# Performance work log

Hardware: AMD Instinct MI355X
Metric: run time of the kernel (lower is better)

Reference implementation:

```python
import jax, jax.numpy as jnp
import numpy as np

B, N, F_IN, F_OUT = 8, 2048, 256, 128
ALPHA = 0.2  # LeakyReLU negative slope
NEG_BIG = -9e15


def setup_inputs() -> dict:
    key = jax.random.key(0)
    k1, k2, k3, k4 = jax.random.split(key, 4)
    h = jax.random.normal(k1, (B, N, F_IN), dtype=jnp.float32)
    adj = jax.random.randint(k2, (B, N, N), 0, 2, dtype=jnp.int32)
    W = jax.random.normal(k3, (F_IN, F_OUT), dtype=jnp.float32) * 0.05
    a = jax.random.normal(k4, (2 * F_OUT,), dtype=jnp.float32) * 0.05
    return {"h": h, "adj": adj, "W": W, "a": a}


def reference(h, adj, W, a):
    # Wh: [B, N, F_OUT]
    Wh = jnp.einsum("bnf,fo->bno", h, W)
    # a([Wh_i || Wh_j]) decomposes: e_ij = a1.Wh_i + a2.Wh_j  (avoids [B,N*N,2F] tensor)
    a1, a2 = a[:F_OUT], a[F_OUT:]
    s1 = jnp.einsum("bno,o->bn", Wh, a1)  # [B, N]
    s2 = jnp.einsum("bno,o->bn", Wh, a2)  # [B, N]
    e = jax.nn.leaky_relu(s1[:, :, None] + s2[:, None, :], negative_slope=ALPHA)  # [B,N,N]
    e = jnp.where(adj > 0, e, NEG_BIG)
    attention = jax.nn.softmax(e, axis=2)
    # dropout is identity (eval / p=0)
    h_prime = jnp.einsum("bij,bjo->bio", attention, Wh)  # [B, N, F_OUT]
    return h_prime
```

## Files before the change

kernel.cpp:

```cpp
#include <hip/hip_runtime.h>

#define NB 8
#define NN 2048
#define FIN 256
#define FOUT 128

typedef __attribute__((ext_vector_type(8))) short short8;
typedef __attribute__((ext_vector_type(4))) float f32x4;

static __device__ __forceinline__ unsigned short f2bf(float f) {
    unsigned int u = __float_as_uint(f);
    u += 0x7fffu + ((u >> 16) & 1u);
    return (unsigned short)(u >> 16);
}

#define BAR_LGKM()                                            \
    do {                                                      \
        asm volatile("s_waitcnt lgkmcnt(0)" ::: "memory");    \
        __builtin_amdgcn_sched_barrier(0);                    \
        __builtin_amdgcn_s_barrier();                         \
        __builtin_amdgcn_sched_barrier(0);                    \
    } while (0)

__global__ __launch_bounds__(256) void gat_prep(
    const float* __restrict__ h, const float* __restrict__ W, const float* __restrict__ a,
    unsigned short* __restrict__ whpv, float* __restrict__ s1g, float* __restrict__ s2g)
{
    __shared__ __align__(16) float hT[64 * FIN];
    __shared__ __align__(16) unsigned short pvs[8192];
    const int t = threadIdx.x;
    const int bx = blockIdx.x;
    const int b = bx >> 5;
    const int jt = bx & 31;
    const int j0 = jt * 64;

    const float* hsrc = h + ((size_t)b * NN + j0) * FIN;
    #pragma unroll
    for (int p = 0; p < 16; ++p) {
        int idx = p * 256 + t;
        *(f32x4*)&hT[idx * 4] = *(const f32x4*)&hsrc[idx * 4];
    }
    __syncthreads();

    const int cg = t & 31;
    const int rg = t >> 5;
    float acc[8][4];
    #pragma unroll
    for (int r = 0; r < 8; ++r)
        #pragma unroll
        for (int q = 0; q < 4; ++q) acc[r][q] = 0.f;

    for (int f = 0; f < FIN; f += 4) {
        f32x4 wv[4];
        #pragma unroll
        for (int q = 0; q < 4; ++q) wv[q] = *(const f32x4*)&W[(f + q) * FOUT + cg * 4];
        #pragma unroll
        for (int r = 0; r < 8; ++r) {
            f32x4 hv = *(const f32x4*)&hT[(rg * 8 + r) * FIN + f];
            #pragma unroll
            for (int q = 0; q < 4; ++q) {
                acc[r][0] += hv[q] * wv[q][0];
                acc[r][1] += hv[q] * wv[q][1];
                acc[r][2] += hv[q] * wv[q][2];
                acc[r][3] += hv[q] * wv[q][3];
            }
        }
    }

    f32x4 a1v = *(const f32x4*)&a[cg * 4];
    f32x4 a2v = *(const f32x4*)&a[FOUT + cg * 4];
    #pragma unroll
    for (int r = 0; r < 8; ++r) {
        float p1 = acc[r][0]*a1v[0] + acc[r][1]*a1v[1] + acc[r][2]*a1v[2] + acc[r][3]*a1v[3];
        float p2 = acc[r][0]*a2v[0] + acc[r][1]*a2v[1] + acc[r][2]*a2v[2] + acc[r][3]*a2v[3];
        #pragma unroll
        for (int m = 16; m >= 1; m >>= 1) {
            p1 += __shfl_xor(p1, m, 64);
            p2 += __shfl_xor(p2, m, 64);
        }
        if (cg == 0) {
            s1g[b * NN + j0 + rg * 8 + r] = p1;
            s2g[b * NN + j0 + rg * 8 + r] = p2;
        }
    }

    #pragma unroll
    for (int r = 0; r < 8; ++r) {
        int jl = rg * 8 + r;
        int kt = jl >> 5, j5 = jl & 31, g = j5 >> 3, i = j5 & 7;
        #pragma unroll
        for (int q = 0; q < 4; ++q) {
            int c = cg * 4 + q;
            int lane = g * 16 + (c & 15);
            int nt = c >> 4;
            pvs[((kt * 8 + nt) * 64 + lane) * 8 + i] = f2bf(acc[r][q]);
        }
    }
    __syncthreads();
    unsigned short* dst = whpv + (size_t)(b * 32 + jt) * 8192;
    #pragma unroll
    for (int p = 0; p < 4; ++p) {
        int idx = p * 2048 + t * 8;
        *(short8*)&dst[idx] = *(const short8*)&pvs[idx];
    }
}

__global__ __launch_bounds__(512, 4) void gat_main(
    const int* __restrict__ adj, const unsigned short* __restrict__ whpv,
    const float* __restrict__ s1g, const float* __restrict__ s2g, float* __restrict__ out)
{
    __shared__ __align__(16) char Plds[2][32 * 128];
    __shared__ __align__(16) unsigned short BL[2][8192];
    __shared__ float Sden[32];

    const int t = threadIdx.x;
    const int bx = blockIdx.x;
    const int b = bx & 7;
    const int i0 = (bx >> 3) * 32;

    const int r  = t >> 4;
    const int jq = t & 15;

    const int lane = t & 63;
    const int w = t >> 6;
    const int mt = w & 1;
    const int nb = w >> 1;
    const int arow = mt * 16 + (lane & 15);
    const int g = lane >> 4;

    const float s1v = s1g[b * NN + i0 + r];

    f32x4 acc[2];
    acc[0] = (f32x4){0.f, 0.f, 0.f, 0.f};
    acc[1] = (f32x4){0.f, 0.f, 0.f, 0.f};
    float ssum = 0.f;

    const int* adjb = adj + (size_t)b * NN * NN + (size_t)i0 * NN;
    const int* aptr = adjb + (size_t)r * NN + jq * 4;
    const unsigned short* whb = whpv + (size_t)b * 32 * 8192;
    const float* s2b = s2g + b * NN;

    int4   ac[2];
    short8 wf0[2], wf1[2];
    f32x4  s2r[2];
    ac[0]  = *(const int4*)aptr;
    wf0[0] = *(const short8*)&whb[t * 8];
    wf1[0] = *(const short8*)&whb[4096 + t * 8];
    s2r[0] = *(const f32x4*)&s2b[jq * 4];
    ac[1]  = *(const int4*)(aptr + 64);
    wf0[1] = *(const short8*)&whb[8192 + t * 8];
    wf1[1] = *(const short8*)&whb[8192 + 4096 + t * 8];
    s2r[1] = *(const f32x4*)&s2b[64 + jq * 4];

    const int pbyte = r * 128 + ((jq >> 1) ^ (r & 7)) * 16 + (jq & 1) * 8;
    const int abyte = arow * 128;

    #pragma unroll 2
    for (int jc = 0; jc < 32; ++jc) {
        const int slot = jc & 1;
        const int buf  = jc & 1;

        int4   a_  = ac[slot];
        short8 wc0 = wf0[slot];
        short8 wc1 = wf1[slot];
        f32x4  s2v = s2r[slot];

        const int jn = (jc + 2) & 31;
        ac[slot]  = *(const int4*)(aptr + jn * 64);
        wf0[slot] = *(const short8*)&whb[(size_t)jn * 8192 + t * 8];
        wf1[slot] = *(const short8*)&whb[(size_t)jn * 8192 + 4096 + t * 8];
        s2r[slot] = *(const f32x4*)&s2b[jn * 64 + jq * 4];

        float p0, p1, p2, p3;
        {
            float e0 = s1v + s2v[0]; e0 = fmaxf(e0, 0.2f * e0);
            p0 = (a_.x > 0) ? __expf(e0) : 0.f;
            float e1 = s1v + s2v[1]; e1 = fmaxf(e1, 0.2f * e1);
            p1 = (a_.y > 0) ? __expf(e1) : 0.f;
            float e2 = s1v + s2v[2]; e2 = fmaxf(e2, 0.2f * e2);
            p2 = (a_.z > 0) ? __expf(e2) : 0.f;
            float e3 = s1v + s2v[3]; e3 = fmaxf(e3, 0.2f * e3);
            p3 = (a_.w > 0) ? __expf(e3) : 0.f;
        }
        ssum += (p0 + p1) + (p2 + p3);
        unsigned int pk0 = (unsigned int)f2bf(p0) | ((unsigned int)f2bf(p1) << 16);
        unsigned int pk1 = (unsigned int)f2bf(p2) | ((unsigned int)f2bf(p3) << 16);
        uint2 pk = {pk0, pk1};
        *(uint2*)&Plds[buf][pbyte] = pk;

        *(short8*)&BL[buf][t * 8] = wc0;
        *(short8*)&BL[buf][4096 + t * 8] = wc1;

        BAR_LGKM();

        #pragma unroll
        for (int kt = 0; kt < 2; ++kt) {
            int aslot = (4 * kt + g) ^ (arow & 7);
            short8 af = *(const short8*)&Plds[buf][abyte + aslot * 16];
            #pragma unroll
            for (int n = 0; n < 2; ++n) {
                int nt = nb * 2 + n;
                short8 bfr = *(const short8*)&BL[buf][((kt * 8 + nt) * 64 + lane) * 8];
                acc[n] = __builtin_amdgcn_mfma_f32_16x16x32_bf16(af, bfr, acc[n], 0, 0, 0);
            }
        }
    }

    {
        float v = ssum;
        #pragma unroll
        for (int m = 8; m >= 1; m >>= 1) v += __shfl_xor(v, m, 64);
        if (jq == 0) Sden[r] = v;
    }
    __syncthreads();

    float* ob = out + ((size_t)b * NN + i0) * FOUT;
    #pragma unroll
    for (int n = 0; n < 2; ++n) {
        int col = (nb * 2 + n) * 16 + (lane & 15);
        #pragma unroll
        for (int q = 0; q < 4; ++q) {
            int row = mt * 16 + (lane >> 4) * 4 + q;
            ob[(size_t)row * FOUT + col] = acc[n][q] / Sden[row];
        }
    }
}

extern "C" void kernel_launch(void* const* d_in, const int* in_sizes, int n_in,
                              void* d_out, int out_size, void* d_ws, size_t ws_size,
                              hipStream_t stream) {
    (void)in_sizes; (void)n_in; (void)out_size; (void)ws_size;
    const float* h   = (const float*)d_in[0];
    const int*   adj = (const int*)d_in[1];
    const float* W   = (const float*)d_in[2];
    const float* a   = (const float*)d_in[3];
    float* out = (float*)d_out;

    unsigned short* whpv = (unsigned short*)d_ws;
    float* s1g = (float*)((char*)d_ws + (4u << 20));
    float* s2g = (float*)((char*)d_ws + (4u << 20) + (64u << 10));

    gat_prep<<<dim3(256), dim3(256), 0, stream>>>(h, W, a, whpv, s1g, s2g);
    gat_main<<<dim3(512), dim3(512), 0, stream>>>(adj, whpv, s1g, s2g, out);
}
```

Measured before the change: 63.76 us.

## Pack adjacency into bitmask in a separate pass and feed Wh fragments directly

Adds an adj2bit kernel that turns the int32 adjacency matrix into a per-row bitmask using wave ballots. The main kernel then reads one 32-bit word per chunk instead of int4 adjacency values. The main kernel also drops LDS staging of Wh: each wave loads its B fragment straight from global memory and computes both 16-row tiles for its 16 output columns. The full adjacency is still read once per call, now in the extra pass, so this adds a launch and a 4 MB bitmask write and read in exchange for a lighter main loop.

New measurement: 80.18 us. 25.8% more time.

```diff
diff --git a/kernel.cpp b/kernel.cpp
--- a/kernel.cpp
+++ b/kernel.cpp
@@ -21,6 +21,31 @@
         __builtin_amdgcn_s_barrier();                         \
         __builtin_amdgcn_sched_barrier(0);                    \
     } while (0)
+
+__global__ __launch_bounds__(256) void adj2bit(
+    const int* __restrict__ adj, unsigned long long* __restrict__ bm)
+{
+    const int t = threadIdx.x;
+    const int lane = t & 63;
+    const int wid = blockIdx.x * 4 + (t >> 6);
+    #pragma unroll 1
+    for (int s = wid; s < 131072; s += 8192) {
+        const size_t base = (size_t)(s >> 3) * NN + (size_t)(s & 7) * 256;
+        int a0 = adj[base + 0 * 64 + lane];
+        int a1 = adj[base + 1 * 64 + lane];
+        int a2 = adj[base + 2 * 64 + lane];
+        int a3 = adj[base + 3 * 64 + lane];
+        unsigned long long b0 = __ballot(a0 > 0);
+        unsigned long long b1 = __ballot(a1 > 0);
+        unsigned long long b2 = __ballot(a2 > 0);
+        unsigned long long b3 = __ballot(a3 > 0);
+        unsigned long long v = b0;
+        v = (lane == 1) ? b1 : v;
+        v = (lane == 2) ? b2 : v;
+        v = (lane == 3) ? b3 : v;
+        if (lane < 4) bm[(size_t)(s >> 3) * 32 + (s & 7) * 4 + lane] = v;
+    }
+}
 
 __global__ __launch_bounds__(256) void gat_prep(
     const float* __restrict__ h, const float* __restrict__ W, const float* __restrict__ a,
@@ -106,11 +131,10 @@
 }
 
 __global__ __launch_bounds__(512, 4) void gat_main(
-    const int* __restrict__ adj, const unsigned short* __restrict__ whpv,
+    const unsigned int* __restrict__ bm32, const unsigned short* __restrict__ whpv,
     const float* __restrict__ s1g, const float* __restrict__ s2g, float* __restrict__ out)
 {
     __shared__ __align__(16) char Plds[2][32 * 128];
-    __shared__ __align__(16) unsigned short BL[2][8192];
     __shared__ float Sden[32];
 
     const int t = threadIdx.x;
@@ -123,86 +147,79 @@
 
     const int lane = t & 63;
     const int w = t >> 6;
-    const int mt = w & 1;
-    const int nb = w >> 1;
-    const int arow = mt * 16 + (lane & 15);
     const int g = lane >> 4;
+    const int c15 = lane & 15;
 
     const float s1v = s1g[b * NN + i0 + r];
 
-    f32x4 acc[2];
-    acc[0] = (f32x4){0.f, 0.f, 0.f, 0.f};
-    acc[1] = (f32x4){0.f, 0.f, 0.f, 0.f};
+    f32x4 acc0 = (f32x4){0.f, 0.f, 0.f, 0.f};
+    f32x4 acc1 = (f32x4){0.f, 0.f, 0.f, 0.f};
     float ssum = 0.f;
 
-    const int* adjb = adj + (size_t)b * NN * NN + (size_t)i0 * NN;
-    const int* aptr = adjb + (size_t)r * NN + jq * 4;
     const unsigned short* whb = whpv + (size_t)b * 32 * 8192;
     const float* s2b = s2g + b * NN;
-
-    int4   ac[2];
-    short8 wf0[2], wf1[2];
-    f32x4  s2r[2];
-    ac[0]  = *(const int4*)aptr;
-    wf0[0] = *(const short8*)&whb[t * 8];
-    wf1[0] = *(const short8*)&whb[4096 + t * 8];
+    const unsigned int* bmr = bm32 + ((size_t)b * NN + i0 + r) * 64 + (jq >> 3);
+    const int jqs = (jq & 7) * 4;
+
+    const unsigned short* wb0 = whb + ((size_t)(0 * 8 + w) * 64 + lane) * 8;
+    const unsigned short* wb1 = whb + ((size_t)(1 * 8 + w) * 64 + lane) * 8;
+
+    unsigned int bmv[2];
+    short8 bp0[2], bp1[2];
+    f32x4 s2r[2];
+    bmv[0] = bmr[0];
+    bmv[1] = bmr[2];
+    bp0[0] = *(const short8*)wb0;
+    bp1[0] = *(const short8*)wb1;
+    bp0[1] = *(const short8*)(wb0 + 8192);
+    bp1[1] = *(const short8*)(wb1 + 8192);
     s2r[0] = *(const f32x4*)&s2b[jq * 4];
-    ac[1]  = *(const int4*)(aptr + 64);
-    wf0[1] = *(const short8*)&whb[8192 + t * 8];
-    wf1[1] = *(const short8*)&whb[8192 + 4096 + t * 8];
     s2r[1] = *(const f32x4*)&s2b[64 + jq * 4];
 
     const int pbyte = r * 128 + ((jq >> 1) ^ (r & 7)) * 16 + (jq & 1) * 8;
-    const int abyte = arow * 128;
+    const int arow0 = c15;
+    const int arow1 = 16 + c15;
 
     #pragma unroll 2
     for (int jc = 0; jc < 32; ++jc) {
         const int slot = jc & 1;
-        const int buf  = jc & 1;
-
-        int4   a_  = ac[slot];
-        short8 wc0 = wf0[slot];
-        short8 wc1 = wf1[slot];
-        f32x4  s2v = s2r[slot];
+
+        unsigned int bw = bmv[slot];
+        short8 f0 = bp0[slot];
+        short8 f1 = bp1[slot];
+        f32x4 s2v = s2r[slot];
 
         const int jn = (jc + 2) & 31;
-        ac[slot]  = *(const int4*)(aptr + jn * 64);
-        wf0[slot] = *(const short8*)&whb[(size_t)jn * 8192 + t * 8];
-        wf1[slot] = *(const short8*)&whb[(size_t)jn * 8192 + 4096 + t * 8];
+        bmv[slot] = bmr[jn * 2];
+        bp0[slot] = *(const short8*)(wb0 + (size_t)jn * 8192);
+        bp1[slot] = *(const short8*)(wb1 + (size_t)jn * 8192);
         s2r[slot] = *(const f32x4*)&s2b[jn * 64 + jq * 4];
 
-        float p0, p1, p2, p3;
-        {
-            float e0 = s1v + s2v[0]; e0 = fmaxf(e0, 0.2f * e0);
-            p0 = (a_.x > 0) ? __expf(e0) : 0.f;
-            float e1 = s1v + s2v[1]; e1 = fmaxf(e1, 0.2f * e1);
-            p1 = (a_.y > 0) ? __expf(e1) : 0.f;
-            float e2 = s1v + s2v[2]; e2 = fmaxf(e2, 0.2f * e2);
-            p2 = (a_.z > 0) ? __expf(e2) : 0.f;
-            float e3 = s1v + s2v[3]; e3 = fmaxf(e3, 0.2f * e3);
-            p3 = (a_.w > 0) ? __expf(e3) : 0.f;
-        }
+        const unsigned int nib = bw >> jqs;
+        float e0 = s1v + s2v[0]; e0 = fmaxf(e0, 0.2f * e0);
+        float p0 = (nib & 1u) ? __expf(e0) : 0.f;
+        float e1 = s1v + s2v[1]; e1 = fmaxf(e1, 0.2f * e1);
+        float p1 = (nib & 2u) ? __expf(e1) : 0.f;
+        float e2 = s1v + s2v[2]; e2 = fmaxf(e2, 0.2f * e2);
+        float p2 = (nib & 4u) ? __expf(e2) : 0.f;
+        float e3 = s1v + s2v[3]; e3 = fmaxf(e3, 0.2f * e3);
+        float p3 = (nib & 8u) ? __expf(e3) : 0.f;
         ssum += (p0 + p1) + (p2 + p3);
         unsigned int pk0 = (unsigned int)f2bf(p0) | ((unsigned int)f2bf(p1) << 16);
         unsigned int pk1 = (unsigned int)f2bf(p2) | ((unsigned int)f2bf(p3) << 16);
         uint2 pk = {pk0, pk1};
-        *(uint2*)&Plds[buf][pbyte] = pk;
-
-        *(short8*)&BL[buf][t * 8] = wc0;
-        *(short8*)&BL[buf][4096 + t * 8] = wc1;
+        *(uint2*)&Plds[slot][pbyte] = pk;
 
         BAR_LGKM();
 
         #pragma unroll
         for (int kt = 0; kt < 2; ++kt) {
-            int aslot = (4 * kt + g) ^ (arow & 7);
-            short8 af = *(const short8*)&Plds[buf][abyte + aslot * 16];
-            #pragma unroll
-            for (int n = 0; n < 2; ++n) {
-                int nt = nb * 2 + n;
-                short8 bfr = *(const short8*)&BL[buf][((kt * 8 + nt) * 64 + lane) * 8];
-                acc[n] = __builtin_amdgcn_mfma_f32_16x16x32_bf16(af, bfr, acc[n], 0, 0, 0);
-            }
+            const int sl = (4 * kt + g) ^ (arow0 & 7);
+            short8 af0 = *(const short8*)&Plds[slot][arow0 * 128 + sl * 16];
+            short8 af1 = *(const short8*)&Plds[slot][arow1 * 128 + sl * 16];
+            short8 bfr = kt ? f1 : f0;
+            acc0 = __builtin_amdgcn_mfma_f32_16x16x32_bf16(af0, bfr, acc0, 0, 0, 0);
+            acc1 = __builtin_amdgcn_mfma_f32_16x16x32_bf16(af1, bfr, acc1, 0, 0, 0);
         }
     }
 
@@ -215,14 +232,13 @@
     __syncthreads();
 
     float* ob = out + ((size_t)b * NN + i0) * FOUT;
-    #pragma unroll
-    for (int n = 0; n < 2; ++n) {
-        int col = (nb * 2 + n) * 16 + (lane & 15);
-        #pragma unroll
-        for (int q = 0; q < 4; ++q) {
-            int row = mt * 16 + (lane >> 4) * 4 + q;
-            ob[(size_t)row * FOUT + col] = acc[n][q] / Sden[row];
-        }
+    const int col = w * 16 + c15;
+    #pragma unroll
+    for (int q = 0; q < 4; ++q) {
+        int row0 = g * 4 + q;
+        int row1 = 16 + g * 4 + q;
+        ob[(size_t)row0 * FOUT + col] = acc0[q] / Sden[row0];
+        ob[(size_t)row1 * FOUT + col] = acc1[q] / Sden[row1];
     }
 }
 
@@ -239,7 +255,9 @@
     unsigned short* whpv = (unsigned short*)d_ws;
     float* s1g = (float*)((char*)d_ws + (4u << 20));
     float* s2g = (float*)((char*)d_ws + (4u << 20) + (64u << 10));
-
+    unsigned long long* bm = (unsigned long long*)((char*)d_ws + (8u << 20));
+
+    adj2bit<<<dim3(2048), dim3(256), 0, stream>>>(adj, bm);
     gat_prep<<<dim3(256), dim3(256), 0, stream>>>(h, W, a, whpv, s1g, s2g);
-    gat_main<<<dim3(512), dim3(512), 0, stream>>>(adj, whpv, s1g, s2g, out);
-}
+    gat_main<<<dim3(512), dim3(512), 0, stream>>>((const unsigned int*)bm, whpv, s1g, s2g, out);
+}
```
